# Kernel tuning notes

Hardware: AMD Instinct MI355X
Metric: run time of the kernel (lower is better)

The kernel has to match this reference:

```python
import math
import jax, jax.numpy as jnp
import numpy as np

B, D, C = 2, 1024, 512          # (b*f with f=1), spatial tokens, channels
H, DH = 8, 64                   # heads, head dim (H*DH == C)
P = 32                          # past length == temporal_max_len
MAX_LEN = 32
HID = max(128, C // 2)          # refiner hidden

def make_pe():
    # sinusoidal APE buffer, shape [MAX_LEN, C]
    position = np.arange(MAX_LEN)[:, None].astype(np.float32)
    div_term = np.exp(np.arange(0, C, 2).astype(np.float32) * (-math.log(10000.0) / C))
    pe = np.zeros((MAX_LEN, C), dtype=np.float32)
    pe[:, 0::2] = np.sin(position * div_term)
    pe[:, 1::2] = np.cos(position * div_term)
    return jnp.asarray(pe)

def setup_inputs() -> dict:
    key = jax.random.key(0)
    ks = jax.random.split(key, 12)
    sc = 0.02
    return {
        "hidden_states": jax.random.normal(ks[0], (B, D, C), jnp.float32),
        "cached_hidden_states": jax.random.normal(ks[1], (B * D, P, C), jnp.float32),
        "Wq": jax.random.normal(ks[2], (C, C), jnp.float32) * sc,
        "Wk": jax.random.normal(ks[3], (C, C), jnp.float32) * sc,
        "Wv": jax.random.normal(ks[4], (C, C), jnp.float32) * sc,
        "Wo": jax.random.normal(ks[5], (C, C), jnp.float32) * sc,
        "bo": jnp.zeros((C,), jnp.float32),
        "W1": jax.random.normal(ks[6], (3 * C, HID), jnp.float32) * sc,
        "b1": jnp.zeros((HID,), jnp.float32),
        "W2": jax.random.normal(ks[7], (HID, 2 * C + 2), jnp.float32) * sc,
        "b2": jnp.zeros((2 * C + 2,), jnp.float32),
        "pe": make_pe(),
        "select_top_r": 8,
    }

def reference(hidden_states, cached_hidden_states, Wq, Wk, Wv, Wo, bo, W1, b1, W2, b2, pe, select_top_r):
    b, d, c = hidden_states.shape
    B0 = b * d
    # '(b f) d c -> (b d) f c' with f=1
    now = hidden_states.reshape(B0, 1, c)
    past = cached_hidden_states                      # [B0, P, C]
    # APE positional encoding
    now_pos = now + pe[:1][None]
    past_pos = past + pe[: past.shape[1]][None]
    # projections (no bias, diffusers CrossAttention style)
    q_now = now_pos @ Wq                             # [B0, 1, C]
    k_now = now_pos @ Wk
    v_now = now_pos @ Wv
    k_past = past_pos @ Wk                           # [B0, P, C]
    v_past = past_pos @ Wv
    # top-r key selection over past
    score = jnp.einsum('bqc,bpc->bqp', q_now, k_past)[:, 0]   # [B0, P]
    _, idx = jax.lax.top_k(score, select_top_r)               # [B0, R]
    k_sel = jnp.take_along_axis(k_past, idx[:, :, None], axis=1)  # [B0, R, C]
    v_sel = jnp.take_along_axis(v_past, idx[:, :, None], axis=1)
    # refiner MLP: concat(q, k, v) -> hidden -> 2C+2
    R = k_sel.shape[1]
    q_rep = jnp.broadcast_to(q_now, (B0, R, c))
    inp = jnp.concatenate([q_rep, k_sel, v_sel], axis=-1)     # [B0, R, 3C]
    h = jax.nn.gelu(inp @ W1 + b1, approximate=False)
    out = h @ W2 + b2                                         # [B0, R, 2C+2]
    dK, dV, log_s, logit_g = jnp.split(out, [c, 2 * c, 2 * c + 1], axis=-1)
    s = jax.nn.softplus(log_s) + 1e-5
    g = jax.nn.sigmoid(logit_g)
    k_sel = k_sel + g * dK * s
    v_sel = v_sel + g * dV * s
    # attention over [selected past ; now]
    key_ = jnp.concatenate([k_sel, k_now], axis=1)            # [B0, R+1, C]
    val_ = jnp.concatenate([v_sel, v_now], axis=1)
    L = key_.shape[1]
    qh = q_now.reshape(B0, 1, H, DH)
    kh = key_.reshape(B0, L, H, DH)
    vh = val_.reshape(B0, L, H, DH)
    scale = DH ** -0.5
    logits = jnp.einsum('bqhd,bkhd->bhqk', qh, kh) * scale
    attn = jax.nn.softmax(logits, axis=-1)
    ctx = jnp.einsum('bhqk,bkhd->bqhd', attn, vh).reshape(B0, 1, c)
    out_proj = ctx @ Wo + bo                                  # [B0, 1, C]
    # '(b d) f c -> (b f) d c' with f=1
    return out_proj.reshape(b, d, c)
```

## Files before the change

### kernel.cpp

```cpp
#include <hip/hip_runtime.h>
#include <math.h>


typedef __attribute__((ext_vector_type(8))) __bf16 bf16x8;
typedef __attribute__((ext_vector_type(4))) float f32x4;
typedef unsigned short u16;
typedef unsigned int u32;

static __device__ __forceinline__ float4 ld4(const float* p) { return *(const float4*)p; }
static __device__ __forceinline__ float gelu_exact(float x) {
  return 0.5f * x * (1.0f + erff(x * 0.70710678118654752f));
}
static __device__ __forceinline__ u16 f2bf(float f) {
  u32 u = __float_as_uint(f);
  u = (u + 0x7fffu + ((u >> 16) & 1u)) >> 16;
  return (u16)u;
}
static __device__ __forceinline__ float bf2f(u16 h) {
  return __uint_as_float(((u32)h) << 16);
}
static __device__ __forceinline__ u32 pk2(float a, float b) {
  return (u32)f2bf(a) | ((u32)f2bf(b) << 16);
}
static __device__ __forceinline__ void gld16(const void* g, void* l) {
  __builtin_amdgcn_global_load_lds((const __attribute__((address_space(1))) void*)g,
                                   (__attribute__((address_space(3))) void*)l, 16, 0, 0);
}

__global__ __launch_bounds__(256) void prep_w(
    const float* __restrict__ Wq, const float* __restrict__ Wk,
    const float* __restrict__ Wv, const float* __restrict__ W1,
    const float* __restrict__ W2, const float* __restrict__ Wo,
    u16* __restrict__ Wqkvt, u16* __restrict__ W1t,
    u16* __restrict__ W2t, u16* __restrict__ Wot) {
  __shared__ float t[32][33];
  const int b = blockIdx.x;
  const float* S; u16* D; int lds_, Kd, nx, t0;
  if (b < 256)       { S = Wq; D = Wqkvt;              lds_ = 512;  Kd = 512;  nx = 16; t0 = 0; }
  else if (b < 512)  { S = Wk; D = Wqkvt + 512 * 512;  lds_ = 512;  Kd = 512;  nx = 16; t0 = 256; }
  else if (b < 768)  { S = Wv; D = Wqkvt + 1024 * 512; lds_ = 512;  Kd = 512;  nx = 16; t0 = 512; }
  else if (b < 1152) { S = W1; D = W1t;                lds_ = 256;  Kd = 1536; nx = 8;  t0 = 768; }
  else if (b < 1408) { S = W2; D = W2t;                lds_ = 1026; Kd = 256;  nx = 32; t0 = 1152; }
  else               { S = Wo; D = Wot;                lds_ = 512;  Kd = 512;  nx = 16; t0 = 1408; }
  const int tile = b - t0;
  const int n0 = (tile % nx) << 5, k0 = (tile / nx) << 5;
  const int tx = threadIdx.x & 31, ty8 = threadIdx.x >> 5;
  for (int yy = ty8; yy < 32; yy += 8)
    t[yy][tx] = S[(size_t)(k0 + yy) * lds_ + n0 + tx];
  __syncthreads();
  for (int yy = ty8; yy < 32; yy += 8)
    D[(size_t)(n0 + yy) * Kd + k0 + tx] = f2bf(t[tx][yy]);
}

__global__ __launch_bounds__(256) void wqk_kernel(const float* __restrict__ Wq,
                                                  const float* __restrict__ Wk,
                                                  float* __restrict__ Wqk) {
  __shared__ float Aq[32][36];
  __shared__ float Bk[32][36];
  const int tid = threadIdx.x;
  const int c0 = blockIdx.y << 5, j0 = blockIdx.x << 5;
  const int r = tid >> 3, ic = (tid & 7) << 2;
  const int ty = tid >> 4, tx = tid & 15;
  float acc00 = 0.f, acc01 = 0.f, acc10 = 0.f, acc11 = 0.f;
  for (int i0 = 0; i0 < 512; i0 += 32) {
    float4 a = ld4(Wq + (size_t)(c0 + r) * 512 + i0 + ic);
    float4 b = ld4(Wk + (size_t)(j0 + r) * 512 + i0 + ic);
    Aq[r][ic] = a.x; Aq[r][ic + 1] = a.y; Aq[r][ic + 2] = a.z; Aq[r][ic + 3] = a.w;
    Bk[r][ic] = b.x; Bk[r][ic + 1] = b.y; Bk[r][ic + 2] = b.z; Bk[r][ic + 3] = b.w;
    __syncthreads();
#pragma unroll
    for (int i = 0; i < 32; ++i) {
      float a0 = Aq[ty * 2][i], a1 = Aq[ty * 2 + 1][i];
      float b0 = Bk[tx * 2][i], b1 = Bk[tx * 2 + 1][i];
      acc00 += a0 * b0; acc01 += a0 * b1; acc10 += a1 * b0; acc11 += a1 * b1;
    }
    __syncthreads();
  }
  Wqk[(size_t)(c0 + ty * 2) * 512 + j0 + tx * 2]     = acc00;
  Wqk[(size_t)(c0 + ty * 2) * 512 + j0 + tx * 2 + 1] = acc01;
  Wqk[(size_t)(c0 + ty * 2 + 1) * 512 + j0 + tx * 2]     = acc10;
  Wqk[(size_t)(c0 + ty * 2 + 1) * 512 + j0 + tx * 2 + 1] = acc11;
}

__global__ __launch_bounds__(256) void qk_gemm(const float* __restrict__ A,
                                               const float* __restrict__ B,
                                               float* __restrict__ C,
                                               const float* __restrict__ pe) {
  __shared__ float As[16][68];
  __shared__ float Bs[16][68];
  const int tid = threadIdx.x;
  const int rm = blockIdx.y << 6, cn = blockIdx.x << 6;
  const int tx = tid & 15, ty = tid >> 4;
  const int ar = tid >> 2, ak = (tid & 3) << 2;
  const int bk = tid >> 4, bn = (tid & 15) << 2;
  const float* Ap = A + (size_t)(rm + ar) * 512;
  float acc[4][4] = {};
  for (int kt = 0; kt < 32; ++kt) {
    const int k0 = (kt << 4) + ak;
    float4 x = ld4(Ap + k0);
    float4 p4 = ld4(pe + k0);
    As[ak + 0][ar] = x.x + p4.x; As[ak + 1][ar] = x.y + p4.y;
    As[ak + 2][ar] = x.z + p4.z; As[ak + 3][ar] = x.w + p4.w;
    *(float4*)&Bs[bk][bn] = ld4(B + (size_t)((kt << 4) + bk) * 512 + cn + bn);
    __syncthreads();
#pragma unroll
    for (int kk = 0; kk < 16; ++kk) {
      float4 a = *(const float4*)&As[kk][ty << 2];
      float4 b = *(const float4*)&Bs[kk][tx << 2];
      acc[0][0] += a.x * b.x; acc[0][1] += a.x * b.y; acc[0][2] += a.x * b.z; acc[0][3] += a.x * b.w;
      acc[1][0] += a.y * b.x; acc[1][1] += a.y * b.y; acc[1][2] += a.y * b.z; acc[1][3] += a.y * b.w;
      acc[2][0] += a.z * b.x; acc[2][1] += a.z * b.y; acc[2][2] += a.z * b.z; acc[2][3] += a.z * b.w;
      acc[3][0] += a.w * b.x; acc[3][1] += a.w * b.y; acc[3][2] += a.w * b.z; acc[3][3] += a.w * b.w;
    }
    __syncthreads();
  }
  const int row0 = rm + (ty << 2), col0 = cn + (tx << 2);
#pragma unroll
  for (int i = 0; i < 4; ++i)
    *(float4*)(C + (size_t)(row0 + i) * 512 + col0) =
        make_float4(acc[i][0], acc[i][1], acc[i][2], acc[i][3]);
}

__global__ __launch_bounds__(256) void score_topk(const float* __restrict__ QK,
                                                  const float* __restrict__ cached,
                                                  const float* __restrict__ pe,
                                                  int* __restrict__ idxv) {
  __shared__ float sc[32];
  const int b0 = blockIdx.x;
  const int tid = threadIdx.x;
  const int wave = tid >> 6, lane = tid & 63;
  const int off = lane << 3;
  const float* qk = QK + (size_t)b0 * 512;
  float4 q0 = ld4(qk + off);
  float4 q1 = ld4(qk + off + 4);
  for (int i = 0; i < 8; ++i) {
    const int p = (wave << 3) + i;
    const float* cp = cached + ((size_t)b0 * 32 + p) * 512 + off;
    const float* pp = pe + (size_t)p * 512 + off;
    float4 c0 = ld4(cp), c1 = ld4(cp + 4);
    float4 e0 = ld4(pp), e1 = ld4(pp + 4);
    float s = (c0.x + e0.x) * q0.x + (c0.y + e0.y) * q0.y +
              (c0.z + e0.z) * q0.z + (c0.w + e0.w) * q0.w +
              (c1.x + e1.x) * q1.x + (c1.y + e1.y) * q1.y +
              (c1.z + e1.z) * q1.z + (c1.w + e1.w) * q1.w;
#pragma unroll
    for (int d = 32; d > 0; d >>= 1) s += __shfl_xor(s, d);
    if (lane == 0) sc[p] = s;
  }
  __syncthreads();
  if (tid == 0) {
    for (int r = 0; r < 8; ++r) {
      float best = -INFINITY; int bi = 0;
      for (int p = 0; p < 32; ++p) {
        float v = sc[p];
        if (v > best) { best = v; bi = p; }
      }
      idxv[b0 * 8 + r] = b0 * 32 + bi;
      sc[bi] = -INFINITY;
    }
  }
}

__global__ __launch_bounds__(256) void prep_a(const float* __restrict__ hidden,
                                              const float* __restrict__ cached,
                                              const float* __restrict__ pe,
                                              const int* __restrict__ idxv,
                                              u16* __restrict__ xh,
                                              u16* __restrict__ gsel) {
  const int row = (blockIdx.x << 2) + (threadIdx.x >> 6);
  const int lane = threadIdx.x & 63;
  const int off = lane << 3;
  const float* src; const float* ps; u16* dst;
  if (row < 2048) {
    src = hidden + (size_t)row * 512; ps = pe; dst = xh + (size_t)row * 512;
  } else {
    const int m = row - 2048;
    const int g = idxv[m];
    src = cached + (size_t)g * 512;
    ps = pe + (size_t)(g & 31) * 512;
    dst = gsel + (size_t)m * 512;
  }
  float4 a = ld4(src + off), b = ld4(src + off + 4);
  float4 p = ld4(ps + off), q = ld4(ps + off + 4);
  int4 o;
  o.x = pk2(a.x + p.x, a.y + p.y);
  o.y = pk2(a.z + p.z, a.w + p.w);
  o.z = pk2(b.x + q.x, b.y + q.y);
  o.w = pk2(b.z + q.z, b.w + q.w);
  *(int4*)(dst + off) = o;
}

template <int CAT, int EP>
__global__ __launch_bounds__(256) void bgemm(
    const u16* __restrict__ Ah, const u16* __restrict__ Ah2,
    const u16* __restrict__ Bt,
    float* __restrict__ Cf, u16* __restrict__ Ch,
    const float* __restrict__ bias, const float* __restrict__ sgv,
    const int K, const int ldc) {
  __shared__ u16 As[4096];
  __shared__ u16 Bs[4096];
  const int tid = threadIdx.x, lane = tid & 63, w = tid >> 6;
  const int rm = blockIdx.y << 7, cn = blockIdx.x << 7;
  const int srow = tid >> 2, skoff = (tid & 3) << 3;

  const u16 *a0, *a1, *q0 = nullptr, *q1 = nullptr;
  if constexpr (CAT == 0) {
    a0 = Ah + (size_t)(rm + srow) * K + skoff;
    a1 = Ah + (size_t)(rm + 64 + srow) * K + skoff;
  } else {
    const int m0 = rm + srow, m1 = rm + 64 + srow;
    q0 = Ah + (size_t)(m0 >> 3) * 512 + skoff;
    q1 = Ah + (size_t)(m1 >> 3) * 512 + skoff;
    a0 = Ah2 + (size_t)m0 * 1024 + skoff;
    a1 = Ah2 + (size_t)m1 * 1024 + skoff;
  }
  const u16* b0 = Bt + (size_t)(cn + srow) * K + skoff;
  const u16* b1 = Bt + (size_t)(cn + 64 + srow) * K + skoff;

  u16* aD0 = As + (w << 9); u16* aD1 = As + 2048 + (w << 9);
  u16* bD0 = Bs + (w << 9); u16* bD1 = Bs + 2048 + (w << 9);
  const int arb = ((((w >> 1) << 6) + (lane & 15)) << 5) + ((lane >> 4) << 3);
  const int brb = ((((w & 1) << 6) + (lane & 15)) << 5) + ((lane >> 4) << 3);

  f32x4 acc[4][4];
#pragma unroll
  for (int i = 0; i < 4; ++i)
#pragma unroll
    for (int j = 0; j < 4; ++j) acc[i][j] = (f32x4){0.f, 0.f, 0.f, 0.f};

  const int nk = K >> 5;
  for (int kt = 0; kt < nk; ++kt) {
    const int ko = kt << 5;
    if (kt) __syncthreads();
    if constexpr (CAT == 0) {
      gld16(a0 + ko, aD0); gld16(a1 + ko, aD1);
    } else {
      if (kt < 16) { gld16(q0 + ko, aD0); gld16(q1 + ko, aD1); }
      else         { gld16(a0 + ko - 512, aD0); gld16(a1 + ko - 512, aD1); }
    }
    gld16(b0 + ko, bD0); gld16(b1 + ko, bD1);
    __syncthreads();
    bf16x8 av[4], bv[4];
#pragma unroll
    for (int i = 0; i < 4; ++i) av[i] = *(const bf16x8*)(As + arb + (i << 9));
#pragma unroll
    for (int j = 0; j < 4; ++j) bv[j] = *(const bf16x8*)(Bs + brb + (j << 9));
#pragma unroll
    for (int i = 0; i < 4; ++i)
#pragma unroll
      for (int j = 0; j < 4; ++j)
        acc[i][j] = __builtin_amdgcn_mfma_f32_16x16x32_bf16(av[i], bv[j], acc[i][j], 0, 0, 0);
  }

  const int row0 = rm + ((w >> 1) << 6) + ((lane >> 4) << 2);
  const int col0 = cn + ((w & 1) << 6) + (lane & 15);
#pragma unroll
  for (int j = 0; j < 4; ++j) {
    const int col = col0 + (j << 4);
    float bcol = 0.f;
    if constexpr (EP == 2 || EP == 3 || EP == 4) bcol = bias[col];
#pragma unroll
    for (int i = 0; i < 4; ++i) {
#pragma unroll
      for (int r = 0; r < 4; ++r) {
        const int rr = row0 + (i << 4) + r;
        const float v = acc[i][j][r];
        if constexpr (EP == 0) {
          Cf[(size_t)rr * ldc + col] = v;
          if (col < 512) Ch[(size_t)rr * 512 + col] = f2bf(v);
        } else if constexpr (EP == 1) {
          Cf[(size_t)rr * ldc + col] = v;
          Ch[(size_t)rr * ldc + col] = f2bf(v);
        } else if constexpr (EP == 2) {
          Ch[(size_t)rr * ldc + col] = f2bf(gelu_exact(v + bcol));
        } else if constexpr (EP == 3) {
          const float s = sgv[2 * rr], g = sgv[2 * rr + 1];
          Cf[(size_t)rr * ldc + col] += g * s * (v + bcol);
        } else {
          Cf[(size_t)rr * ldc + col] = v + bcol;
        }
      }
    }
  }
}

__global__ __launch_bounds__(256) void sg_kernel(const u16* __restrict__ hb,
                                                 const float* __restrict__ W2,
                                                 const float* __restrict__ b2,
                                                 float* __restrict__ sgv) {
  __shared__ float w0[256], w1[256];
  const int tid = threadIdx.x;
  w0[tid] = W2[(size_t)tid * 1026 + 1024];
  w1[tid] = W2[(size_t)tid * 1026 + 1025];
  __syncthreads();
  const int wave = tid >> 6, lane = tid & 63;
  const int m = (blockIdx.x << 2) + wave;
  const int k4 = lane << 2;
  ushort4 hv = *(const ushort4*)(hb + (size_t)m * 256 + k4);
  const float h0 = bf2f(hv.x), h1 = bf2f(hv.y), h2 = bf2f(hv.z), h3 = bf2f(hv.w);
  float a0 = h0 * w0[k4] + h1 * w0[k4 + 1] + h2 * w0[k4 + 2] + h3 * w0[k4 + 3];
  float a1 = h0 * w1[k4] + h1 * w1[k4 + 1] + h2 * w1[k4 + 2] + h3 * w1[k4 + 3];
#pragma unroll
  for (int d = 32; d > 0; d >>= 1) { a0 += __shfl_xor(a0, d); a1 += __shfl_xor(a1, d); }
  if (lane == 0) {
    float t0 = a0 + b2[1024];
    float t1 = a1 + b2[1025];
    float s = (t0 > 0.f ? t0 + log1pf(expf(-t0)) : log1pf(expf(t0))) + 1e-5f;
    float g = 1.f / (1.f + expf(-t1));
    sgv[m * 2] = s; sgv[m * 2 + 1] = g;
  }
}

__global__ __launch_bounds__(256) void attn2(const float* __restrict__ Yf,
                                             const float* __restrict__ kvf,
                                             u16* __restrict__ ctxh) {
  const int w = threadIdx.x >> 6, lane = threadIdx.x & 63;
  const int b0 = (blockIdx.x << 2) + w;
  const int off = lane << 3;
  const float* yr = Yf + (size_t)b0 * 1536;
  float4 qa = ld4(yr + off), qb = ld4(yr + off + 4);
  float lg[9];
#pragma unroll
  for (int k = 0; k < 9; ++k) {
    const float* kr = (k < 8) ? (kvf + (size_t)(b0 * 8 + k) * 1024 + off)
                              : (yr + 512 + off);
    float4 ka = ld4(kr), kb = ld4(kr + 4);
    float s = qa.x * ka.x + qa.y * ka.y + qa.z * ka.z + qa.w * ka.w +
              qb.x * kb.x + qb.y * kb.y + qb.z * kb.z + qb.w * kb.w;
    s += __shfl_xor(s, 1); s += __shfl_xor(s, 2); s += __shfl_xor(s, 4);
    lg[k] = s * 0.125f;
  }
  float m = lg[0];
#pragma unroll
  for (int k = 1; k < 9; ++k) m = fmaxf(m, lg[k]);
  float sum = 0.f;
#pragma unroll
  for (int k = 0; k < 9; ++k) { lg[k] = expf(lg[k] - m); sum += lg[k]; }
  const float inv = 1.f / sum;
  float c[8] = {0.f, 0.f, 0.f, 0.f, 0.f, 0.f, 0.f, 0.f};
#pragma unroll
  for (int k = 0; k < 9; ++k) {
    const float* vr = (k < 8) ? (kvf + (size_t)(b0 * 8 + k) * 1024 + 512 + off)
                              : (yr + 1024 + off);
    float4 va = ld4(vr), vb = ld4(vr + 4);
    const float wk = lg[k] * inv;
    c[0] += wk * va.x; c[1] += wk * va.y; c[2] += wk * va.z; c[3] += wk * va.w;
    c[4] += wk * vb.x; c[5] += wk * vb.y; c[6] += wk * vb.z; c[7] += wk * vb.w;
  }
  int4 o;
  o.x = pk2(c[0], c[1]); o.y = pk2(c[2], c[3]);
  o.z = pk2(c[4], c[5]); o.w = pk2(c[6], c[7]);
  *(int4*)(ctxh + (size_t)b0 * 512 + off) = o;
}

extern "C" void kernel_launch(void* const* d_in, const int* in_sizes, int n_in,
                              void* d_out, int out_size, void* d_ws, size_t ws_size,
                              hipStream_t stream) {
  const float* hidden = (const float*)d_in[0];
  const float* cached = (const float*)d_in[1];
  const float* Wq = (const float*)d_in[2];
  const float* Wk = (const float*)d_in[3];
  const float* Wv = (const float*)d_in[4];
  const float* Wo = (const float*)d_in[5];
  const float* bo = (const float*)d_in[6];
  const float* W1 = (const float*)d_in[7];
  const float* b1 = (const float*)d_in[8];
  const float* W2 = (const float*)d_in[9];
  const float* b2 = (const float*)d_in[10];
  const float* pe = (const float*)d_in[11];

  float* ws = (float*)d_ws;
  float* Wqk = ws;
  float* qkb = Wqk + 262144;
  float* Yf  = qkb + 1048576;
  float* kvf = Yf + 3145728;
  float* sgv = kvf + 16777216;
  int* idxv  = (int*)(sgv + 32768);
  u16* Wqkvt = (u16*)(idxv + 16384);
  u16* W1t   = Wqkvt + 786432;
  u16* W2t   = W1t + 393216;
  u16* Wot   = W2t + 262144;
  u16* xh    = Wot + 262144;
  u16* gsel  = xh + 1048576;
  u16* qh    = gsel + 8388608;
  u16* kvh   = qh + 1048576;
  u16* hb    = kvh + 16777216;
  u16* ctxh  = hb + 4194304;
  float* out = (float*)d_out;
  (void)in_sizes; (void)n_in; (void)out_size; (void)ws_size;

  prep_w<<<dim3(1664), 256, 0, stream>>>(Wq, Wk, Wv, W1, W2, Wo, Wqkvt, W1t, W2t, Wot);
  wqk_kernel<<<dim3(16, 16), 256, 0, stream>>>(Wq, Wk, Wqk);
  qk_gemm<<<dim3(8, 32), 256, 0, stream>>>(hidden, Wqk, qkb, pe);
  score_topk<<<dim3(2048), 256, 0, stream>>>(qkb, cached, pe, idxv);
  prep_a<<<dim3(4608), 256, 0, stream>>>(hidden, cached, pe, idxv, xh, gsel);
  bgemm<0, 0><<<dim3(12, 16), 256, 0, stream>>>(xh, nullptr, Wqkvt, Yf, qh,
                                                nullptr, nullptr, 512, 1536);
  bgemm<0, 1><<<dim3(8, 128), 256, 0, stream>>>(gsel, nullptr, Wqkvt + 512 * 512, kvf, kvh,
                                                nullptr, nullptr, 512, 1024);
  bgemm<1, 2><<<dim3(2, 128), 256, 0, stream>>>(qh, kvh, W1t, nullptr, hb,
                                                b1, nullptr, 1536, 256);
  sg_kernel<<<dim3(4096), 256, 0, stream>>>(hb, W2, b2, sgv);
  bgemm<0, 3><<<dim3(8, 128), 256, 0, stream>>>(hb, nullptr, W2t, kvf, nullptr,
                                                b2, sgv, 256, 1024);
  attn2<<<dim3(512), 256, 0, stream>>>(Yf, kvf, ctxh);
  bgemm<0, 4><<<dim3(4, 16), 256, 0, stream>>>(ctxh, nullptr, Wot, out, nullptr,
                                               bo, nullptr, 512, 512);
}
```

Measured before the change: 493.3 us.

## Fuse pipeline into fewer kernels and keep intermediates in bf16

Merges weight prep with the Wq·Wk product, folds the top-r gather into the scoring kernel, and runs the Q/KV projection GEMMs as a single launch. The sigmoid/softplus head is folded into the first MLP GEMM, and the delta update is applied in place on bf16 K/V. Y and K/V now stay in bf16 only, with no fp32 copies, which cuts launch count and memory traffic. The cost is extra bf16 rounding of the refined K/V and of q, plus a 64-row MLP tile that may leave the GPU with low occupancy.

```diff
diff --git a/kernel.cpp b/kernel.cpp
--- a/kernel.cpp
+++ b/kernel.cpp
@@ -22,64 +22,71 @@
 static __device__ __forceinline__ u32 pk2(float a, float b) {
   return (u32)f2bf(a) | ((u32)f2bf(b) << 16);
 }
+static __device__ __forceinline__ void ld8bf(const u16* p, float* o) {
+  int4 v = *(const int4*)p;
+  o[0] = bf2f((u16)((u32)v.x & 0xffffu)); o[1] = bf2f((u16)(((u32)v.x) >> 16));
+  o[2] = bf2f((u16)((u32)v.y & 0xffffu)); o[3] = bf2f((u16)(((u32)v.y) >> 16));
+  o[4] = bf2f((u16)((u32)v.z & 0xffffu)); o[5] = bf2f((u16)(((u32)v.z) >> 16));
+  o[6] = bf2f((u16)((u32)v.w & 0xffffu)); o[7] = bf2f((u16)(((u32)v.w) >> 16));
+}
 static __device__ __forceinline__ void gld16(const void* g, void* l) {
   __builtin_amdgcn_global_load_lds((const __attribute__((address_space(1))) void*)g,
                                    (__attribute__((address_space(3))) void*)l, 16, 0, 0);
 }
 
-__global__ __launch_bounds__(256) void prep_w(
+__global__ __launch_bounds__(256) void prep_all(
     const float* __restrict__ Wq, const float* __restrict__ Wk,
     const float* __restrict__ Wv, const float* __restrict__ W1,
     const float* __restrict__ W2, const float* __restrict__ Wo,
     u16* __restrict__ Wqkvt, u16* __restrict__ W1t,
-    u16* __restrict__ W2t, u16* __restrict__ Wot) {
-  __shared__ float t[32][33];
+    u16* __restrict__ W2t, u16* __restrict__ Wot,
+    float* __restrict__ Wqk) {
   const int b = blockIdx.x;
-  const float* S; u16* D; int lds_, Kd, nx, t0;
-  if (b < 256)       { S = Wq; D = Wqkvt;              lds_ = 512;  Kd = 512;  nx = 16; t0 = 0; }
-  else if (b < 512)  { S = Wk; D = Wqkvt + 512 * 512;  lds_ = 512;  Kd = 512;  nx = 16; t0 = 256; }
-  else if (b < 768)  { S = Wv; D = Wqkvt + 1024 * 512; lds_ = 512;  Kd = 512;  nx = 16; t0 = 512; }
-  else if (b < 1152) { S = W1; D = W1t;                lds_ = 256;  Kd = 1536; nx = 8;  t0 = 768; }
-  else if (b < 1408) { S = W2; D = W2t;                lds_ = 1026; Kd = 256;  nx = 32; t0 = 1152; }
-  else               { S = Wo; D = Wot;                lds_ = 512;  Kd = 512;  nx = 16; t0 = 1408; }
-  const int tile = b - t0;
-  const int n0 = (tile % nx) << 5, k0 = (tile / nx) << 5;
-  const int tx = threadIdx.x & 31, ty8 = threadIdx.x >> 5;
-  for (int yy = ty8; yy < 32; yy += 8)
-    t[yy][tx] = S[(size_t)(k0 + yy) * lds_ + n0 + tx];
-  __syncthreads();
-  for (int yy = ty8; yy < 32; yy += 8)
-    D[(size_t)(n0 + yy) * Kd + k0 + tx] = f2bf(t[tx][yy]);
-}
-
-__global__ __launch_bounds__(256) void wqk_kernel(const float* __restrict__ Wq,
-                                                  const float* __restrict__ Wk,
-                                                  float* __restrict__ Wqk) {
-  __shared__ float Aq[32][36];
-  __shared__ float Bk[32][36];
-  const int tid = threadIdx.x;
-  const int c0 = blockIdx.y << 5, j0 = blockIdx.x << 5;
-  const int r = tid >> 3, ic = (tid & 7) << 2;
-  const int ty = tid >> 4, tx = tid & 15;
-  float acc00 = 0.f, acc01 = 0.f, acc10 = 0.f, acc11 = 0.f;
-  for (int i0 = 0; i0 < 512; i0 += 32) {
-    float4 a = ld4(Wq + (size_t)(c0 + r) * 512 + i0 + ic);
-    float4 b = ld4(Wk + (size_t)(j0 + r) * 512 + i0 + ic);
-    Aq[r][ic] = a.x; Aq[r][ic + 1] = a.y; Aq[r][ic + 2] = a.z; Aq[r][ic + 3] = a.w;
-    Bk[r][ic] = b.x; Bk[r][ic + 1] = b.y; Bk[r][ic + 2] = b.z; Bk[r][ic + 3] = b.w;
-    __syncthreads();
-#pragma unroll
-    for (int i = 0; i < 32; ++i) {
-      float a0 = Aq[ty * 2][i], a1 = Aq[ty * 2 + 1][i];
-      float b0 = Bk[tx * 2][i], b1 = Bk[tx * 2 + 1][i];
-      acc00 += a0 * b0; acc01 += a0 * b1; acc10 += a1 * b0; acc11 += a1 * b1;
+  if (b < 1664) {
+    __shared__ float t[32][33];
+    const float* S; u16* D; int lds_, Kd, nx, t0;
+    if (b < 256)       { S = Wq; D = Wqkvt;              lds_ = 512;  Kd = 512;  nx = 16; t0 = 0; }
+    else if (b < 512)  { S = Wk; D = Wqkvt + 512 * 512;  lds_ = 512;  Kd = 512;  nx = 16; t0 = 256; }
+    else if (b < 768)  { S = Wv; D = Wqkvt + 1024 * 512; lds_ = 512;  Kd = 512;  nx = 16; t0 = 512; }
+    else if (b < 1152) { S = W1; D = W1t;                lds_ = 256;  Kd = 1536; nx = 8;  t0 = 768; }
+    else if (b < 1408) { S = W2; D = W2t;                lds_ = 1026; Kd = 256;  nx = 32; t0 = 1152; }
+    else               { S = Wo; D = Wot;                lds_ = 512;  Kd = 512;  nx = 16; t0 = 1408; }
+    const int tile = b - t0;
+    const int n0 = (tile % nx) << 5, k0 = (tile / nx) << 5;
+    const int tx = threadIdx.x & 31, ty8 = threadIdx.x >> 5;
+    for (int yy = ty8; yy < 32; yy += 8)
+      t[yy][tx] = S[(size_t)(k0 + yy) * lds_ + n0 + tx];
+    __syncthreads();
+    for (int yy = ty8; yy < 32; yy += 8)
+      D[(size_t)(n0 + yy) * Kd + k0 + tx] = f2bf(t[tx][yy]);
+  } else {
+    __shared__ float Aq[32][36];
+    __shared__ float Bk[32][36];
+    const int tile = b - 1664;
+    const int c0 = (tile >> 4) << 5, j0 = (tile & 15) << 5;
+    const int tid = threadIdx.x;
+    const int r = tid >> 3, ic = (tid & 7) << 2;
+    const int ty = tid >> 4, tx = tid & 15;
+    float a00 = 0.f, a01 = 0.f, a10 = 0.f, a11 = 0.f;
+    for (int i0 = 0; i0 < 512; i0 += 32) {
+      float4 a = ld4(Wq + (size_t)(c0 + r) * 512 + i0 + ic);
+      float4 bb = ld4(Wk + (size_t)(j0 + r) * 512 + i0 + ic);
+      Aq[r][ic] = a.x; Aq[r][ic + 1] = a.y; Aq[r][ic + 2] = a.z; Aq[r][ic + 3] = a.w;
+      Bk[r][ic] = bb.x; Bk[r][ic + 1] = bb.y; Bk[r][ic + 2] = bb.z; Bk[r][ic + 3] = bb.w;
+      __syncthreads();
+#pragma unroll
+      for (int i = 0; i < 32; ++i) {
+        float x0 = Aq[ty * 2][i], x1 = Aq[ty * 2 + 1][i];
+        float y0 = Bk[tx * 2][i], y1 = Bk[tx * 2 + 1][i];
+        a00 += x0 * y0; a01 += x0 * y1; a10 += x1 * y0; a11 += x1 * y1;
+      }
+      __syncthreads();
     }
-    __syncthreads();
-  }
-  Wqk[(size_t)(c0 + ty * 2) * 512 + j0 + tx * 2]     = acc00;
-  Wqk[(size_t)(c0 + ty * 2) * 512 + j0 + tx * 2 + 1] = acc01;
-  Wqk[(size_t)(c0 + ty * 2 + 1) * 512 + j0 + tx * 2]     = acc10;
-  Wqk[(size_t)(c0 + ty * 2 + 1) * 512 + j0 + tx * 2 + 1] = acc11;
+    Wqk[(size_t)(c0 + ty * 2) * 512 + j0 + tx * 2]         = a00;
+    Wqk[(size_t)(c0 + ty * 2) * 512 + j0 + tx * 2 + 1]     = a01;
+    Wqk[(size_t)(c0 + ty * 2 + 1) * 512 + j0 + tx * 2]     = a10;
+    Wqk[(size_t)(c0 + ty * 2 + 1) * 512 + j0 + tx * 2 + 1] = a11;
+  }
 }
 
 __global__ __launch_bounds__(256) void qk_gemm(const float* __restrict__ A,
@@ -121,20 +128,21 @@
         make_float4(acc[i][0], acc[i][1], acc[i][2], acc[i][3]);
 }
 
-__global__ __launch_bounds__(256) void score_topk(const float* __restrict__ QK,
-                                                  const float* __restrict__ cached,
-                                                  const float* __restrict__ pe,
-                                                  int* __restrict__ idxv) {
+__global__ __launch_bounds__(256) void score_topk_gather(
+    const float* __restrict__ QK, const float* __restrict__ cached,
+    const float* __restrict__ pe, const float* __restrict__ hidden,
+    u16* __restrict__ xh, u16* __restrict__ gsel) {
   __shared__ float sc[32];
+  __shared__ int ix[8];
   const int b0 = blockIdx.x;
   const int tid = threadIdx.x;
-  const int wave = tid >> 6, lane = tid & 63;
+  const int w = tid >> 6, lane = tid & 63;
   const int off = lane << 3;
   const float* qk = QK + (size_t)b0 * 512;
   float4 q0 = ld4(qk + off);
   float4 q1 = ld4(qk + off + 4);
   for (int i = 0; i < 8; ++i) {
-    const int p = (wave << 3) + i;
+    const int p = (w << 3) + i;
     const float* cp = cached + ((size_t)b0 * 32 + p) * 512 + off;
     const float* pp = pe + (size_t)p * 512 + off;
     float4 c0 = ld4(cp), c1 = ld4(cp + 4);
@@ -155,89 +163,212 @@
         float v = sc[p];
         if (v > best) { best = v; bi = p; }
       }
-      idxv[b0 * 8 + r] = b0 * 32 + bi;
+      ix[r] = bi;
       sc[bi] = -INFINITY;
     }
   }
-}
-
-__global__ __launch_bounds__(256) void prep_a(const float* __restrict__ hidden,
-                                              const float* __restrict__ cached,
-                                              const float* __restrict__ pe,
-                                              const int* __restrict__ idxv,
-                                              u16* __restrict__ xh,
-                                              u16* __restrict__ gsel) {
-  const int row = (blockIdx.x << 2) + (threadIdx.x >> 6);
-  const int lane = threadIdx.x & 63;
-  const int off = lane << 3;
-  const float* src; const float* ps; u16* dst;
-  if (row < 2048) {
-    src = hidden + (size_t)row * 512; ps = pe; dst = xh + (size_t)row * 512;
+  __syncthreads();
+#pragma unroll
+  for (int rr = 0; rr < 2; ++rr) {
+    const int rsel = w + (rr << 2);
+    const int p = ix[rsel];
+    const float* cp = cached + ((size_t)b0 * 32 + p) * 512 + off;
+    const float* pp = pe + (size_t)p * 512 + off;
+    float4 c0 = ld4(cp), c1 = ld4(cp + 4);
+    float4 e0 = ld4(pp), e1 = ld4(pp + 4);
+    int4 o;
+    o.x = pk2(c0.x + e0.x, c0.y + e0.y);
+    o.y = pk2(c0.z + e0.z, c0.w + e0.w);
+    o.z = pk2(c1.x + e1.x, c1.y + e1.y);
+    o.w = pk2(c1.z + e1.z, c1.w + e1.w);
+    *(int4*)(gsel + (size_t)(b0 * 8 + rsel) * 512 + off) = o;
+  }
+  if (w == 0) {
+    const float* hp = hidden + (size_t)b0 * 512 + off;
+    float4 a = ld4(hp), b = ld4(hp + 4);
+    float4 p0 = ld4(pe + off), p1 = ld4(pe + off + 4);
+    int4 o;
+    o.x = pk2(a.x + p0.x, a.y + p0.y);
+    o.y = pk2(a.z + p0.z, a.w + p0.w);
+    o.z = pk2(b.x + p1.x, b.y + p1.y);
+    o.w = pk2(b.z + p1.z, b.w + p1.w);
+    *(int4*)(xh + (size_t)b0 * 512 + off) = o;
+  }
+}
+
+__global__ __launch_bounds__(256) void bgemm_fused1(
+    const u16* __restrict__ gsel, const u16* __restrict__ xh,
+    const u16* __restrict__ Wqkvt, u16* __restrict__ kvh,
+    u16* __restrict__ Yh) {
+  __shared__ u16 As[4096];
+  __shared__ u16 Bs[4096];
+  const int tid = threadIdx.x, lane = tid & 63, w = tid >> 6;
+  const int bid = blockIdx.x;
+  const int srow = tid >> 2, skoff = (tid & 3) << 3;
+  const u16 *a0, *b0; u16* C; int ldc, rm, cn;
+  if (bid < 1024) {
+    rm = (bid >> 3) << 7; cn = (bid & 7) << 7;
+    a0 = gsel + (size_t)(rm + srow) * 512 + skoff;
+    b0 = Wqkvt + (size_t)(512 + cn + srow) * 512 + skoff;
+    C = kvh; ldc = 1024;
   } else {
-    const int m = row - 2048;
-    const int g = idxv[m];
-    src = cached + (size_t)g * 512;
-    ps = pe + (size_t)(g & 31) * 512;
-    dst = gsel + (size_t)m * 512;
-  }
-  float4 a = ld4(src + off), b = ld4(src + off + 4);
-  float4 p = ld4(ps + off), q = ld4(ps + off + 4);
-  int4 o;
-  o.x = pk2(a.x + p.x, a.y + p.y);
-  o.y = pk2(a.z + p.z, a.w + p.w);
-  o.z = pk2(b.x + q.x, b.y + q.y);
-  o.w = pk2(b.z + q.z, b.w + q.w);
-  *(int4*)(dst + off) = o;
-}
-
-template <int CAT, int EP>
-__global__ __launch_bounds__(256) void bgemm(
-    const u16* __restrict__ Ah, const u16* __restrict__ Ah2,
-    const u16* __restrict__ Bt,
-    float* __restrict__ Cf, u16* __restrict__ Ch,
-    const float* __restrict__ bias, const float* __restrict__ sgv,
-    const int K, const int ldc) {
+    const int b2 = bid - 1024;
+    rm = (b2 / 12) << 7; cn = (b2 % 12) << 7;
+    a0 = xh + (size_t)(rm + srow) * 512 + skoff;
+    b0 = Wqkvt + (size_t)(cn + srow) * 512 + skoff;
+    C = Yh; ldc = 1536;
+  }
+  const u16* a1 = a0 + (size_t)64 * 512;
+  const u16* b1 = b0 + (size_t)64 * 512;
+  u16* aD0 = As + (w << 9); u16* aD1 = As + 2048 + (w << 9);
+  u16* bD0 = Bs + (w << 9); u16* bD1 = Bs + 2048 + (w << 9);
+  const int arb = ((((w >> 1) << 6) + (lane & 15)) << 5) + ((lane >> 4) << 3);
+  const int brb = ((((w & 1) << 6) + (lane & 15)) << 5) + ((lane >> 4) << 3);
+  f32x4 acc[4][4];
+#pragma unroll
+  for (int i = 0; i < 4; ++i)
+#pragma unroll
+    for (int j = 0; j < 4; ++j) acc[i][j] = (f32x4){0.f, 0.f, 0.f, 0.f};
+  for (int kt = 0; kt < 16; ++kt) {
+    const int ko = kt << 5;
+    if (kt) __syncthreads();
+    gld16(a0 + ko, aD0); gld16(a1 + ko, aD1);
+    gld16(b0 + ko, bD0); gld16(b1 + ko, bD1);
+    __syncthreads();
+    bf16x8 av[4], bv[4];
+#pragma unroll
+    for (int i = 0; i < 4; ++i) av[i] = *(const bf16x8*)(As + arb + (i << 9));
+#pragma unroll
+    for (int j = 0; j < 4; ++j) bv[j] = *(const bf16x8*)(Bs + brb + (j << 9));
+#pragma unroll
+    for (int i = 0; i < 4; ++i)
+#pragma unroll
+      for (int j = 0; j < 4; ++j)
+        acc[i][j] = __builtin_amdgcn_mfma_f32_16x16x32_bf16(av[i], bv[j], acc[i][j], 0, 0, 0);
+  }
+  const int row0 = rm + ((w >> 1) << 6) + ((lane >> 4) << 2);
+  const int col0 = cn + ((w & 1) << 6) + (lane & 15);
+#pragma unroll
+  for (int j = 0; j < 4; ++j) {
+    const int col = col0 + (j << 4);
+#pragma unroll
+    for (int i = 0; i < 4; ++i)
+#pragma unroll
+      for (int r = 0; r < 4; ++r)
+        C[(size_t)(row0 + (i << 4) + r) * ldc + col] = f2bf(acc[i][j][r]);
+  }
+}
+
+__global__ __launch_bounds__(256) void mlp1_sg(
+    const u16* __restrict__ Yh, const u16* __restrict__ kvh,
+    const u16* __restrict__ W1t, const float* __restrict__ b1,
+    const float* __restrict__ W2, const float* __restrict__ b2,
+    u16* __restrict__ hb, float* __restrict__ sgv) {
+  __shared__ u16 As[2048];
+  __shared__ u16 Bs[8192];
+  __shared__ float wa[256], wb[256];
+  const int tid = threadIdx.x, lane = tid & 63, w = tid >> 6;
+  const int rm = blockIdx.x << 6;
+  const int srow = tid >> 2, skoff = (tid & 3) << 3;
+  wa[tid] = W2[(size_t)tid * 1026 + 1024];
+  wb[tid] = W2[(size_t)tid * 1026 + 1025];
+  const int m0 = rm + srow;
+  const u16* aq = Yh + (size_t)(m0 >> 3) * 1536 + skoff;
+  const u16* akv = kvh + (size_t)m0 * 1024 + skoff;
+  const u16* bsrc = W1t + (size_t)srow * 1536 + skoff;
+  u16* aD = As + (w << 9);
+  u16* bD0 = Bs + (w << 9);
+  u16* bD1 = Bs + 2048 + (w << 9);
+  u16* bD2 = Bs + 4096 + (w << 9);
+  u16* bD3 = Bs + 6144 + (w << 9);
+  const int arb = ((lane & 15) << 5) + ((lane >> 4) << 3);
+  const int brb = (((w << 6) + (lane & 15)) << 5) + ((lane >> 4) << 3);
+  f32x4 acc[4][4];
+#pragma unroll
+  for (int i = 0; i < 4; ++i)
+#pragma unroll
+    for (int j = 0; j < 4; ++j) acc[i][j] = (f32x4){0.f, 0.f, 0.f, 0.f};
+  for (int kt = 0; kt < 48; ++kt) {
+    const int ko = kt << 5;
+    if (kt) __syncthreads();
+    if (kt < 16) gld16(aq + ko, aD);
+    else         gld16(akv + ko - 512, aD);
+    gld16(bsrc + ko, bD0);
+    gld16(bsrc + (size_t)64 * 1536 + ko, bD1);
+    gld16(bsrc + (size_t)128 * 1536 + ko, bD2);
+    gld16(bsrc + (size_t)192 * 1536 + ko, bD3);
+    __syncthreads();
+    bf16x8 av[4], bv[4];
+#pragma unroll
+    for (int i = 0; i < 4; ++i) av[i] = *(const bf16x8*)(As + arb + (i << 9));
+#pragma unroll
+    for (int j = 0; j < 4; ++j) bv[j] = *(const bf16x8*)(Bs + brb + (j << 9));
+#pragma unroll
+    for (int i = 0; i < 4; ++i)
+#pragma unroll
+      for (int j = 0; j < 4; ++j)
+        acc[i][j] = __builtin_amdgcn_mfma_f32_16x16x32_bf16(av[i], bv[j], acc[i][j], 0, 0, 0);
+  }
+  const int row0 = rm + ((lane >> 4) << 2);
+  const int col0 = (w << 6) + (lane & 15);
+#pragma unroll
+  for (int j = 0; j < 4; ++j) {
+    const int col = col0 + (j << 4);
+    const float bc = b1[col];
+#pragma unroll
+    for (int i = 0; i < 4; ++i)
+#pragma unroll
+      for (int r = 0; r < 4; ++r)
+        hb[(size_t)(row0 + (i << 4) + r) * 256 + col] = f2bf(gelu_exact(acc[i][j][r] + bc));
+  }
+  __syncthreads();
+  const int row = tid >> 2, q = tid & 3;
+  const int rr = rm + row;
+  const u16* hp = hb + (size_t)rr * 256 + (q << 6);
+  float pa = 0.f, pb = 0.f;
+  for (int c = 0; c < 64; c += 8) {
+    float h[8]; ld8bf(hp + c, h);
+    const int cb = (q << 6) + c;
+#pragma unroll
+    for (int t = 0; t < 8; ++t) { pa += h[t] * wa[cb + t]; pb += h[t] * wb[cb + t]; }
+  }
+  pa += __shfl_xor(pa, 1); pa += __shfl_xor(pa, 2);
+  pb += __shfl_xor(pb, 1); pb += __shfl_xor(pb, 2);
+  if (q == 0) {
+    const float t0 = pa + b2[1024];
+    const float t1 = pb + b2[1025];
+    const float s = (t0 > 0.f ? t0 + log1pf(expf(-t0)) : log1pf(expf(t0))) + 1e-5f;
+    const float g = 1.f / (1.f + expf(-t1));
+    sgv[2 * rr] = s; sgv[2 * rr + 1] = g;
+  }
+}
+
+__global__ __launch_bounds__(256) void bgemm_delta(
+    const u16* __restrict__ hb, const u16* __restrict__ W2t,
+    u16* __restrict__ kvh, const float* __restrict__ b2,
+    const float* __restrict__ sgv) {
   __shared__ u16 As[4096];
   __shared__ u16 Bs[4096];
   const int tid = threadIdx.x, lane = tid & 63, w = tid >> 6;
   const int rm = blockIdx.y << 7, cn = blockIdx.x << 7;
   const int srow = tid >> 2, skoff = (tid & 3) << 3;
-
-  const u16 *a0, *a1, *q0 = nullptr, *q1 = nullptr;
-  if constexpr (CAT == 0) {
-    a0 = Ah + (size_t)(rm + srow) * K + skoff;
-    a1 = Ah + (size_t)(rm + 64 + srow) * K + skoff;
-  } else {
-    const int m0 = rm + srow, m1 = rm + 64 + srow;
-    q0 = Ah + (size_t)(m0 >> 3) * 512 + skoff;
-    q1 = Ah + (size_t)(m1 >> 3) * 512 + skoff;
-    a0 = Ah2 + (size_t)m0 * 1024 + skoff;
-    a1 = Ah2 + (size_t)m1 * 1024 + skoff;
-  }
-  const u16* b0 = Bt + (size_t)(cn + srow) * K + skoff;
-  const u16* b1 = Bt + (size_t)(cn + 64 + srow) * K + skoff;
-
+  const u16* a0 = hb + (size_t)(rm + srow) * 256 + skoff;
+  const u16* a1 = a0 + (size_t)64 * 256;
+  const u16* b0 = W2t + (size_t)(cn + srow) * 256 + skoff;
+  const u16* b1 = b0 + (size_t)64 * 256;
   u16* aD0 = As + (w << 9); u16* aD1 = As + 2048 + (w << 9);
   u16* bD0 = Bs + (w << 9); u16* bD1 = Bs + 2048 + (w << 9);
   const int arb = ((((w >> 1) << 6) + (lane & 15)) << 5) + ((lane >> 4) << 3);
   const int brb = ((((w & 1) << 6) + (lane & 15)) << 5) + ((lane >> 4) << 3);
-
   f32x4 acc[4][4];
 #pragma unroll
   for (int i = 0; i < 4; ++i)
 #pragma unroll
     for (int j = 0; j < 4; ++j) acc[i][j] = (f32x4){0.f, 0.f, 0.f, 0.f};
-
-  const int nk = K >> 5;
-  for (int kt = 0; kt < nk; ++kt) {
+  for (int kt = 0; kt < 8; ++kt) {
     const int ko = kt << 5;
     if (kt) __syncthreads();
-    if constexpr (CAT == 0) {
-      gld16(a0 + ko, aD0); gld16(a1 + ko, aD1);
-    } else {
-      if (kt < 16) { gld16(q0 + ko, aD0); gld16(q1 + ko, aD1); }
-      else         { gld16(a0 + ko - 512, aD0); gld16(a1 + ko - 512, aD1); }
-    }
+    gld16(a0 + ko, aD0); gld16(a1 + ko, aD1);
     gld16(b0 + ko, bD0); gld16(b1 + ko, bD1);
     __syncthreads();
     bf16x8 av[4], bv[4];
@@ -251,82 +382,42 @@
       for (int j = 0; j < 4; ++j)
         acc[i][j] = __builtin_amdgcn_mfma_f32_16x16x32_bf16(av[i], bv[j], acc[i][j], 0, 0, 0);
   }
-
   const int row0 = rm + ((w >> 1) << 6) + ((lane >> 4) << 2);
   const int col0 = cn + ((w & 1) << 6) + (lane & 15);
-#pragma unroll
-  for (int j = 0; j < 4; ++j) {
-    const int col = col0 + (j << 4);
-    float bcol = 0.f;
-    if constexpr (EP == 2 || EP == 3 || EP == 4) bcol = bias[col];
-#pragma unroll
-    for (int i = 0; i < 4; ++i) {
-#pragma unroll
-      for (int r = 0; r < 4; ++r) {
-        const int rr = row0 + (i << 4) + r;
-        const float v = acc[i][j][r];
-        if constexpr (EP == 0) {
-          Cf[(size_t)rr * ldc + col] = v;
-          if (col < 512) Ch[(size_t)rr * 512 + col] = f2bf(v);
-        } else if constexpr (EP == 1) {
-          Cf[(size_t)rr * ldc + col] = v;
-          Ch[(size_t)rr * ldc + col] = f2bf(v);
-        } else if constexpr (EP == 2) {
-          Ch[(size_t)rr * ldc + col] = f2bf(gelu_exact(v + bcol));
-        } else if constexpr (EP == 3) {
-          const float s = sgv[2 * rr], g = sgv[2 * rr + 1];
-          Cf[(size_t)rr * ldc + col] += g * s * (v + bcol);
-        } else {
-          Cf[(size_t)rr * ldc + col] = v + bcol;
-        }
+  float bc[4];
+#pragma unroll
+  for (int j = 0; j < 4; ++j) bc[j] = b2[col0 + (j << 4)];
+#pragma unroll
+  for (int i = 0; i < 4; ++i)
+#pragma unroll
+    for (int r = 0; r < 4; ++r) {
+      const int rr = row0 + (i << 4) + r;
+      const float gs = sgv[2 * rr] * sgv[2 * rr + 1];
+      u16* p = kvh + (size_t)rr * 1024 + col0;
+#pragma unroll
+      for (int j = 0; j < 4; ++j) {
+        const int o = j << 4;
+        p[o] = f2bf(bf2f(p[o]) + gs * (acc[i][j][r] + bc[j]));
       }
     }
-  }
-}
-
-__global__ __launch_bounds__(256) void sg_kernel(const u16* __restrict__ hb,
-                                                 const float* __restrict__ W2,
-                                                 const float* __restrict__ b2,
-                                                 float* __restrict__ sgv) {
-  __shared__ float w0[256], w1[256];
-  const int tid = threadIdx.x;
-  w0[tid] = W2[(size_t)tid * 1026 + 1024];
-  w1[tid] = W2[(size_t)tid * 1026 + 1025];
-  __syncthreads();
-  const int wave = tid >> 6, lane = tid & 63;
-  const int m = (blockIdx.x << 2) + wave;
-  const int k4 = lane << 2;
-  ushort4 hv = *(const ushort4*)(hb + (size_t)m * 256 + k4);
-  const float h0 = bf2f(hv.x), h1 = bf2f(hv.y), h2 = bf2f(hv.z), h3 = bf2f(hv.w);
-  float a0 = h0 * w0[k4] + h1 * w0[k4 + 1] + h2 * w0[k4 + 2] + h3 * w0[k4 + 3];
-  float a1 = h0 * w1[k4] + h1 * w1[k4 + 1] + h2 * w1[k4 + 2] + h3 * w1[k4 + 3];
-#pragma unroll
-  for (int d = 32; d > 0; d >>= 1) { a0 += __shfl_xor(a0, d); a1 += __shfl_xor(a1, d); }
-  if (lane == 0) {
-    float t0 = a0 + b2[1024];
-    float t1 = a1 + b2[1025];
-    float s = (t0 > 0.f ? t0 + log1pf(expf(-t0)) : log1pf(expf(t0))) + 1e-5f;
-    float g = 1.f / (1.f + expf(-t1));
-    sgv[m * 2] = s; sgv[m * 2 + 1] = g;
-  }
-}
-
-__global__ __launch_bounds__(256) void attn2(const float* __restrict__ Yf,
-                                             const float* __restrict__ kvf,
+}
+
+__global__ __launch_bounds__(256) void attn2(const u16* __restrict__ Yh,
+                                             const u16* __restrict__ kvh,
                                              u16* __restrict__ ctxh) {
   const int w = threadIdx.x >> 6, lane = threadIdx.x & 63;
   const int b0 = (blockIdx.x << 2) + w;
   const int off = lane << 3;
-  const float* yr = Yf + (size_t)b0 * 1536;
-  float4 qa = ld4(yr + off), qb = ld4(yr + off + 4);
+  const u16* yr = Yh + (size_t)b0 * 1536;
+  float qv[8]; ld8bf(yr + off, qv);
   float lg[9];
 #pragma unroll
   for (int k = 0; k < 9; ++k) {
-    const float* kr = (k < 8) ? (kvf + (size_t)(b0 * 8 + k) * 1024 + off)
-                              : (yr + 512 + off);
-    float4 ka = ld4(kr), kb = ld4(kr + 4);
-    float s = qa.x * ka.x + qa.y * ka.y + qa.z * ka.z + qa.w * ka.w +
-              qb.x * kb.x + qb.y * kb.y + qb.z * kb.z + qb.w * kb.w;
+    const u16* kr = (k < 8) ? (kvh + (size_t)(b0 * 8 + k) * 1024 + off)
+                            : (yr + 512 + off);
+    float kv[8]; ld8bf(kr, kv);
+    float s = qv[0] * kv[0] + qv[1] * kv[1] + qv[2] * kv[2] + qv[3] * kv[3] +
+              qv[4] * kv[4] + qv[5] * kv[5] + qv[6] * kv[6] + qv[7] * kv[7];
     s += __shfl_xor(s, 1); s += __shfl_xor(s, 2); s += __shfl_xor(s, 4);
     lg[k] = s * 0.125f;
   }
@@ -340,17 +431,69 @@
   float c[8] = {0.f, 0.f, 0.f, 0.f, 0.f, 0.f, 0.f, 0.f};
 #pragma unroll
   for (int k = 0; k < 9; ++k) {
-    const float* vr = (k < 8) ? (kvf + (size_t)(b0 * 8 + k) * 1024 + 512 + off)
-                              : (yr + 1024 + off);
-    float4 va = ld4(vr), vb = ld4(vr + 4);
+    const u16* vr = (k < 8) ? (kvh + (size_t)(b0 * 8 + k) * 1024 + 512 + off)
+                            : (yr + 1024 + off);
+    float vv[8]; ld8bf(vr, vv);
     const float wk = lg[k] * inv;
-    c[0] += wk * va.x; c[1] += wk * va.y; c[2] += wk * va.z; c[3] += wk * va.w;
-    c[4] += wk * vb.x; c[5] += wk * vb.y; c[6] += wk * vb.z; c[7] += wk * vb.w;
+#pragma unroll
+    for (int t = 0; t < 8; ++t) c[t] += wk * vv[t];
   }
   int4 o;
   o.x = pk2(c[0], c[1]); o.y = pk2(c[2], c[3]);
   o.z = pk2(c[4], c[5]); o.w = pk2(c[6], c[7]);
   *(int4*)(ctxh + (size_t)b0 * 512 + off) = o;
+}
+
+__global__ __launch_bounds__(256) void bgemm_out(
+    const u16* __restrict__ ctxh, const u16* __restrict__ Wot,
+    float* __restrict__ out, const float* __restrict__ bo) {
+  __shared__ u16 As[4096];
+  __shared__ u16 Bs[4096];
+  const int tid = threadIdx.x, lane = tid & 63, w = tid >> 6;
+  const int rm = blockIdx.y << 7, cn = blockIdx.x << 7;
+  const int srow = tid >> 2, skoff = (tid & 3) << 3;
+  const u16* a0 = ctxh + (size_t)(rm + srow) * 512 + skoff;
+  const u16* a1 = a0 + (size_t)64 * 512;
+  const u16* b0 = Wot + (size_t)(cn + srow) * 512 + skoff;
+  const u16* b1 = b0 + (size_t)64 * 512;
+  u16* aD0 = As + (w << 9); u16* aD1 = As + 2048 + (w << 9);
+  u16* bD0 = Bs + (w << 9); u16* bD1 = Bs + 2048 + (w << 9);
+  const int arb = ((((w >> 1) << 6) + (lane & 15)) << 5) + ((lane >> 4) << 3);
+  const int brb = ((((w & 1) << 6) + (lane & 15)) << 5) + ((lane >> 4) << 3);
+  f32x4 acc[4][4];
+#pragma unroll
+  for (int i = 0; i < 4; ++i)
+#pragma unroll
+    for (int j = 0; j < 4; ++j) acc[i][j] = (f32x4){0.f, 0.f, 0.f, 0.f};
+  for (int kt = 0; kt < 16; ++kt) {
+    const int ko = kt << 5;
+    if (kt) __syncthreads();
+    gld16(a0 + ko, aD0); gld16(a1 + ko, aD1);
+    gld16(b0 + ko, bD0); gld16(b1 + ko, bD1);
+    __syncthreads();
+    bf16x8 av[4], bv[4];
+#pragma unroll
+    for (int i = 0; i < 4; ++i) av[i] = *(const bf16x8*)(As + arb + (i << 9));
+#pragma unroll
+    for (int j = 0; j < 4; ++j) bv[j] = *(const bf16x8*)(Bs + brb + (j << 9));
+#pragma unroll
+    for (int i = 0; i < 4; ++i)
+#pragma unroll
+      for (int j = 0; j < 4; ++j)
+        acc[i][j] = __builtin_amdgcn_mfma_f32_16x16x32_bf16(av[i], bv[j], acc[i][j], 0, 0, 0);
+  }
+  const int row0 = rm + ((w >> 1) << 6) + ((lane >> 4) << 2);
+  const int col0 = cn + ((w & 1) << 6) + (lane & 15);
+  float bc[4];
+#pragma unroll
+  for (int j = 0; j < 4; ++j) bc[j] = bo[col0 + (j << 4)];
+#pragma unroll
+  for (int j = 0; j < 4; ++j)
+#pragma unroll
+    for (int i = 0; i < 4; ++i)
+#pragma unroll
+      for (int r = 0; r < 4; ++r)
+        out[(size_t)(row0 + (i << 4) + r) * 512 + col0 + (j << 4)] = acc[i][j][r] + bc[j];
 }
 
 extern "C" void kernel_launch(void* const* d_in, const int* in_sizes, int n_in,
@@ -372,38 +515,27 @@
   float* ws = (float*)d_ws;
   float* Wqk = ws;
   float* qkb = Wqk + 262144;
-  float* Yf  = qkb + 1048576;
-  float* kvf = Yf + 3145728;
-  float* sgv = kvf + 16777216;
-  int* idxv  = (int*)(sgv + 32768);
-  u16* Wqkvt = (u16*)(idxv + 16384);
+  float* sgv = qkb + 1048576;
+  u16* Wqkvt = (u16*)(sgv + 32768);
   u16* W1t   = Wqkvt + 786432;
   u16* W2t   = W1t + 393216;
   u16* Wot   = W2t + 262144;
   u16* xh    = Wot + 262144;
   u16* gsel  = xh + 1048576;
-  u16* qh    = gsel + 8388608;
-  u16* kvh   = qh + 1048576;
+  u16* Yh    = gsel + 8388608;
+  u16* kvh   = Yh + 3145728;
   u16* hb    = kvh + 16777216;
   u16* ctxh  = hb + 4194304;
   float* out = (float*)d_out;
   (void)in_sizes; (void)n_in; (void)out_size; (void)ws_size;
 
-  prep_w<<<dim3(1664), 256, 0, stream>>>(Wq, Wk, Wv, W1, W2, Wo, Wqkvt, W1t, W2t, Wot);
-  wqk_kernel<<<dim3(16, 16), 256, 0, stream>>>(Wq, Wk, Wqk);
+  prep_all<<<dim3(1920), 256, 0, stream>>>(Wq, Wk, Wv, W1, W2, Wo,
+                                           Wqkvt, W1t, W2t, Wot, Wqk);
   qk_gemm<<<dim3(8, 32), 256, 0, stream>>>(hidden, Wqk, qkb, pe);
-  score_topk<<<dim3(2048), 256, 0, stream>>>(qkb, cached, pe, idxv);
-  prep_a<<<dim3(4608), 256, 0, stream>>>(hidden, cached, pe, idxv, xh, gsel);
-  bgemm<0, 0><<<dim3(12, 16), 256, 0, stream>>>(xh, nullptr, Wqkvt, Yf, qh,
-                                                nullptr, nullptr, 512, 1536);
-  bgemm<0, 1><<<dim3(8, 128), 256, 0, stream>>>(gsel, nullptr, Wqkvt + 512 * 512, kvf, kvh,
-                                                nullptr, nullptr, 512, 1024);
-  bgemm<1, 2><<<dim3(2, 128), 256, 0, stream>>>(qh, kvh, W1t, nullptr, hb,
-                                                b1, nullptr, 1536, 256);
-  sg_kernel<<<dim3(4096), 256, 0, stream>>>(hb, W2, b2, sgv);
-  bgemm<0, 3><<<dim3(8, 128), 256, 0, stream>>>(hb, nullptr, W2t, kvf, nullptr,
-                                                b2, sgv, 256, 1024);
-  attn2<<<dim3(512), 256, 0, stream>>>(Yf, kvf, ctxh);
-  bgemm<0, 4><<<dim3(4, 16), 256, 0, stream>>>(ctxh, nullptr, Wot, out, nullptr,
-                                               bo, nullptr, 512, 512);
-}
+  score_topk_gather<<<dim3(2048), 256, 0, stream>>>(qkb, cached, pe, hidden, xh, gsel);
+  bgemm_fused1<<<dim3(1216), 256, 0, stream>>>(gsel, xh, Wqkvt, kvh, Yh);
+  mlp1_sg<<<dim3(256), 256, 0, stream>>>(Yh, kvh, W1t, b1, W2, b2, hb, sgv);
+  bgemm_delta<<<dim3(8, 128), 256, 0, stream>>>(hb, W2t, kvh, b2, sgv);
+  attn2<<<dim3(512), 256, 0, stream>>>(Yh, kvh, ctxh);
+  bgemm_out<<<dim3(4, 16), 256, 0, stream>>>(ctxh, Wot, out, bo);
+}
```

Measured after the change: 443.0 us. 1.11x faster.
